# Kernel tuning notes

Measured on AMD Instinct MI355X. Metric: run time of the kernel, lower is better.

## Reference

```python
import jax, jax.numpy as jnp
import numpy as np

N_HEADS = 16
ROPE_THETA = 10000.0


def _rotate_half(x):
    d = x.shape[-1] // 2
    return jnp.concatenate([-x[..., d:], x[..., :d]], axis=-1)


def setup_inputs() -> dict:
    key = jax.random.key(0)
    k1, k2, k3, k4 = jax.random.split(key, 4)
    B, S, D = 2, 2048, 2048
    std = 0.02
    return {
        "x": jax.random.normal(k1, (B, S, D), dtype=jnp.float32),
        "wq": std * jax.random.normal(k2, (D, D), dtype=jnp.float32),
        "wkv": std * jax.random.normal(k3, (D, 2 * D), dtype=jnp.float32),
        "wo": std * jax.random.normal(k4, (D, D), dtype=jnp.float32),
    }


def reference(x, wq, wkv, wo):
    # prefill case: kv_cache=None, past_length=0
    B, S, D = x.shape
    H = N_HEADS
    dh = D // H

    Q = x @ wq.T                                   # [B,S,D]
    K, V = jnp.split(x @ wkv, 2, axis=-1)          # [B,S,D] each

    q = Q.reshape(B, S, H, dh).transpose(0, 2, 1, 3)  # [B,H,S,dh]
    k = K.reshape(B, S, H, dh).transpose(0, 2, 1, 3)
    v = V.reshape(B, S, H, dh).transpose(0, 2, 1, 3)

    # RoPE tables (cos/sin of outer(pos, inv_freq), duplicated across halves)
    inv_freq = 1.0 / (ROPE_THETA ** (jnp.arange(0, dh, 2, dtype=jnp.float32) / dh))
    emb = jnp.arange(S, dtype=jnp.float32)[:, None] * inv_freq[None, :]  # [S, dh/2]
    cos = jnp.tile(jnp.cos(emb), (1, 2))[None, None]  # [1,1,S,dh]
    sin = jnp.tile(jnp.sin(emb), (1, 2))[None, None]

    q = q * cos + _rotate_half(q) * sin
    k = k * cos + _rotate_half(k) * sin

    scale = 1.0 / jnp.sqrt(jnp.asarray(dh, dtype=x.dtype))
    scores = jnp.einsum('bhqd,bhkd->bhqk', q, k) * scale  # [B,H,S,S]
    causal = jnp.tril(jnp.ones((S, S), dtype=bool))
    scores = jnp.where(causal[None, None], scores, -jnp.inf)
    attn = jax.nn.softmax(scores, axis=-1)

    out = jnp.einsum('bhqk,bhkd->bhqd', attn, v)          # [B,H,S,dh]
    out = out.transpose(0, 2, 1, 3).reshape(B, S, D)
    return out @ wo.T
```

## Files before the change

kernel.cpp:

```cpp
#include <hip/hip_runtime.h>
#include <stdint.h>

typedef unsigned short u16;
typedef __attribute__((ext_vector_type(8))) short short8;
typedef __attribute__((ext_vector_type(4))) float floatx4;

#define MFMA16(a, b, c) __builtin_amdgcn_mfma_f32_16x16x32_bf16(a, b, c, 0, 0, 0)

static __device__ __forceinline__ void gl_lds16(const void* g, void* l) {
  __builtin_amdgcn_global_load_lds(
      (const __attribute__((address_space(1))) uint32_t*)g,
      (__attribute__((address_space(3))) uint32_t*)l, 16, 0, 0);
}

static __device__ __forceinline__ float b2f(u16 u) {
  union { float f; unsigned u; } v;
  v.u = ((unsigned)u) << 16;
  return v.f;
}
static __device__ __forceinline__ u16 f2b(float f) {
  union { float f; unsigned u; } v;
  v.f = f;
  unsigned r = v.u + 0x7fffu + ((v.u >> 16) & 1u);
  return (u16)(r >> 16);
}

template <int CTRL>
static __device__ __forceinline__ float dppf(float x) {
  return __builtin_bit_cast(
      float, __builtin_amdgcn_update_dpp(0, __builtin_bit_cast(int, x), CTRL,
                                         0xF, 0xF, true));
}
static __device__ __forceinline__ float sum16(float x) {
  x += dppf<0x128>(x);
  x += dppf<0x124>(x);
  x += dppf<0x122>(x);
  x += dppf<0x121>(x);
  return x;
}
static __device__ __forceinline__ float max16(float x) {
  x = fmaxf(x, dppf<0x128>(x));
  x = fmaxf(x, dppf<0x124>(x));
  x = fmaxf(x, dppf<0x122>(x));
  x = fmaxf(x, dppf<0x121>(x));
  return x;
}

__global__ __launch_bounds__(256) void detect_f32(const u16* __restrict__ x,
                                                  int* __restrict__ flag) {
  __shared__ int cnt[256];
  int c = 0;
  for (int i = threadIdx.x; i < 65536; i += 256) {
    int e = (x[i] >> 7) & 0xFF;
    if (e >= 140) ++c;
  }
  cnt[threadIdx.x] = c;
  __syncthreads();
  for (int s = 128; s > 0; s >>= 1) {
    if (threadIdx.x < (unsigned)s) cnt[threadIdx.x] += cnt[threadIdx.x + s];
    __syncthreads();
  }
  if (threadIdx.x == 0) *flag = (cnt[0] > 1000) ? 1 : 0;
}

__global__ __launch_bounds__(256) void convert_in8(const void* __restrict__ src,
                                                   u16* __restrict__ dst, int n8,
                                                   const int* __restrict__ flag) {
  int i = blockIdx.x * 256 + threadIdx.x;
  if (i >= n8) return;
  short8 r;
  if (*flag) {
    const float4* s = (const float4*)src;
    float4 a = s[2 * i], b = s[2 * i + 1];
    r[0] = (short)f2b(a.x); r[1] = (short)f2b(a.y);
    r[2] = (short)f2b(a.z); r[3] = (short)f2b(a.w);
    r[4] = (short)f2b(b.x); r[5] = (short)f2b(b.y);
    r[6] = (short)f2b(b.z); r[7] = (short)f2b(b.w);
  } else {
    r = ((const short8*)src)[i];
  }
  ((short8*)dst)[i] = r;
}

__global__ __launch_bounds__(256) void transpose_conv(const void* __restrict__ in,
                                                      u16* __restrict__ out,
                                                      int R, int Ccols,
                                                      const int* __restrict__ flag) {
  __shared__ u16 tile[32][33];
  int f = *flag;
  int c0 = blockIdx.x * 32, r0 = blockIdx.y * 32;
  int lx = threadIdx.x & 31, ly = threadIdx.x >> 5;
#pragma unroll
  for (int i = 0; i < 32; i += 8) {
    size_t idx = (size_t)(r0 + ly + i) * Ccols + c0 + lx;
    tile[ly + i][lx] = f ? f2b(((const float*)in)[idx]) : ((const u16*)in)[idx];
  }
  __syncthreads();
#pragma unroll
  for (int i = 0; i < 32; i += 8)
    out[(size_t)(c0 + ly + i) * R + r0 + lx] = tile[lx][ly + i];
}

__global__ __launch_bounds__(256) void transpose_v(const u16* __restrict__ KV,
                                                   u16* __restrict__ Vt) {
  __shared__ u16 tile[32][33];
  int b = blockIdx.z;
  int d0 = blockIdx.x * 32, s0 = blockIdx.y * 32;
  int lx = threadIdx.x & 31, ly = threadIdx.x >> 5;
  const u16* src = KV + ((size_t)(b * 2048 + s0)) * 4096 + 2048 + d0;
#pragma unroll
  for (int i = 0; i < 32; i += 8)
    tile[ly + i][lx] = src[(size_t)(ly + i) * 4096 + lx];
  __syncthreads();
  u16* dst = Vt + ((size_t)(b * 2048 + d0)) * 2048 + s0;
#pragma unroll
  for (int i = 0; i < 32; i += 8)
    dst[(size_t)(ly + i) * 2048 + lx] = tile[lx][ly + i];
}

__global__ __launch_bounds__(256) void gemm_nt(const u16* __restrict__ A,
                                               const u16* __restrict__ Bm,
                                               void* __restrict__ Cv,
                                               int M, int N, int K,
                                               const int* __restrict__ flag,
                                               int flag_mode) {
  __shared__ u16 Ash[128 * 64];
  __shared__ u16 Bsh[128 * 64];
  int tid = threadIdx.x, w = tid >> 6, lane = tid & 63;
  int quad = lane >> 4, l15 = lane & 15;
  int m0 = blockIdx.y * 128, n0 = blockIdx.x * 128;
  int wm = (w & 1) * 64, wn = (w >> 1) * 64;
  int f32out = flag_mode ? *flag : 0;

  floatx4 acc[4][4];
#pragma unroll
  for (int i = 0; i < 4; ++i)
#pragma unroll
    for (int j = 0; j < 4; ++j) acc[i][j] = floatx4{0.f, 0.f, 0.f, 0.f};

  int srow = lane >> 3;
  int gch = (lane & 7) ^ srow;
  const u16* Ag = A + (size_t)(m0 + w * 32 + srow) * K + gch * 8;
  const u16* Bg = Bm + (size_t)(n0 + w * 32 + srow) * K + gch * 8;

  for (int k0 = 0; k0 < K; k0 += 64) {
    __syncthreads();
#pragma unroll
    for (int t = 0; t < 4; ++t) {
      gl_lds16(Ag + (size_t)t * 8 * K + k0, (void*)(Ash + (w * 32 + t * 8) * 64));
      gl_lds16(Bg + (size_t)t * 8 * K + k0, (void*)(Bsh + (w * 32 + t * 8) * 64));
    }
    __syncthreads();
#pragma unroll
    for (int kk = 0; kk < 2; ++kk) {
      int c = kk * 4 + quad;
      short8 af[4], bf[4];
#pragma unroll
      for (int i = 0; i < 4; ++i) {
        int m = wm + 16 * i + l15;
        af[i] = *(const short8*)(Ash + m * 64 + ((c ^ (m & 7)) << 3));
        int n = wn + 16 * i + l15;
        bf[i] = *(const short8*)(Bsh + n * 64 + ((c ^ (n & 7)) << 3));
      }
#pragma unroll
      for (int i = 0; i < 4; ++i)
#pragma unroll
        for (int j = 0; j < 4; ++j) acc[i][j] = MFMA16(af[i], bf[j], acc[i][j]);
    }
  }

#pragma unroll
  for (int i = 0; i < 4; ++i)
#pragma unroll
    for (int r = 0; r < 4; ++r) {
      int row = m0 + wm + 16 * i + quad * 4 + r;
      if (f32out) {
        float* cp = (float*)Cv + (size_t)row * N + n0 + wn + l15;
#pragma unroll
        for (int j = 0; j < 4; ++j) cp[16 * j] = acc[i][j][r];
      } else {
        u16* cp = (u16*)Cv + (size_t)row * N + n0 + wn + l15;
#pragma unroll
        for (int j = 0; j < 4; ++j) cp[16 * j] = f2b(acc[i][j][r]);
      }
    }
}

__global__ __launch_bounds__(512, 2) void gemm8(const u16* __restrict__ A,
                                                const u16* __restrict__ Bm,
                                                void* __restrict__ Cv,
                                                int M, int N, int K,
                                                const int* __restrict__ flag,
                                                int flag_mode) {
  __shared__ u16 Ash[2 * 256 * 64];
  __shared__ u16 Bsh[2 * 256 * 64];
  int tid = threadIdx.x, w = tid >> 6, lane = tid & 63;
  int quad = lane >> 4, l15 = lane & 15;
  int wr = w >> 2, wc = w & 3;
  int wm = wr * 128, wn = wc * 64;
  int m0 = blockIdx.y * 256, n0 = blockIdx.x * 256;
  int f32out = flag_mode ? *flag : 0;
  const int NT = K >> 6;

  int srow8 = lane >> 3;
  int gch = (lane & 7) ^ srow8;
  const u16* Ag = A + (size_t)(m0 + w * 8 + srow8) * K + gch * 8;
  const u16* Bg = Bm + (size_t)(n0 + w * 8 + srow8) * K + gch * 8;
  int ldsrow = w * 8;

  floatx4 acc[8][4];
#pragma unroll
  for (int i = 0; i < 8; ++i)
#pragma unroll
    for (int j = 0; j < 4; ++j) acc[i][j] = floatx4{0.f, 0.f, 0.f, 0.f};

  int ch0 = ((quad ^ (l15 & 7)) << 3);
  int ch1 = (((4 + quad) ^ (l15 & 7)) << 3);

  auto stage = [&](int qi) {
    int tau = qi >> 2;
    int tc = tau < NT ? tau : NT - 1;
    int hh = qi & 3;
    int half = (hh & 1) * 128;
    int sbuf = (tau & 1) * (256 * 64);
    size_t kof = (size_t)tc * 64;
    if (hh < 2) {
      gl_lds16(Bg + (size_t)half * K + kof,
               (void*)(Bsh + sbuf + (half + ldsrow) * 64));
      gl_lds16(Bg + (size_t)(half + 64) * K + kof,
               (void*)(Bsh + sbuf + (half + 64 + ldsrow) * 64));
    } else {
      gl_lds16(Ag + (size_t)half * K + kof,
               (void*)(Ash + sbuf + (half + ldsrow) * 64));
      gl_lds16(Ag + (size_t)(half + 64) * K + kof,
               (void*)(Ash + sbuf + (half + 64 + ldsrow) * 64));
    }
  };

  stage(0); stage(1); stage(2); stage(3);
  __asm__ volatile("s_waitcnt vmcnt(4)" ::: "memory");
  stage(4); stage(5); stage(6);
  __asm__ volatile("s_waitcnt vmcnt(6)" ::: "memory");
  __builtin_amdgcn_s_barrier();

  for (int t = 0; t < NT; ++t) {
    u16* As = Ash + (t & 1) * (256 * 64);
    u16* Bs = Bsh + (t & 1) * (256 * 64);
    if (t) {
      __asm__ volatile("s_waitcnt vmcnt(6)" ::: "memory");
      __builtin_amdgcn_s_barrier();
    }
    int qb = 7 + 4 * t;
    short8 bf[8], af0[8], af1[8];

#pragma unroll
    for (int j = 0; j < 4; ++j) {
      int n = wn + 16 * j + l15;
      bf[2 * j] = *(const short8*)(Bs + n * 64 + ch0);
    }
#pragma unroll
    for (int i = 0; i < 4; ++i) {
      int m = wm + 16 * i + l15;
      af0[2 * i] = *(const short8*)(As + m * 64 + ch0);
    }
    stage(qb);
    __builtin_amdgcn_s_barrier();
    __asm__ volatile("s_waitcnt lgkmcnt(0)" ::: "memory");
    __builtin_amdgcn_sched_barrier(0);
    __builtin_amdgcn_s_setprio(1);
#pragma unroll
    for (int i = 0; i < 4; ++i)
#pragma unroll
      for (int j = 0; j < 4; ++j)
        acc[i][j] = MFMA16(af0[2 * i], bf[2 * j], acc[i][j]);
    __builtin_amdgcn_s_setprio(0);
    __builtin_amdgcn_s_barrier();

#pragma unroll
    for (int j = 0; j < 4; ++j) {
      int n = wn + 16 * j + l15;
      bf[2 * j + 1] = *(const short8*)(Bs + n * 64 + ch1);
    }
#pragma unroll
    for (int i = 0; i < 4; ++i) {
      int m = wm + 16 * i + l15;
      af0[2 * i + 1] = *(const short8*)(As + m * 64 + ch1);
    }
    stage(qb + 1);
    __builtin_amdgcn_s_barrier();
    __asm__ volatile("s_waitcnt lgkmcnt(0)" ::: "memory");
    __builtin_amdgcn_sched_barrier(0);
    __builtin_amdgcn_s_setprio(1);
#pragma unroll
    for (int i = 0; i < 4; ++i)
#pragma unroll
      for (int j = 0; j < 4; ++j)
        acc[i][j] = MFMA16(af0[2 * i + 1], bf[2 * j + 1], acc[i][j]);
    __builtin_amdgcn_s_setprio(0);
    __builtin_amdgcn_s_barrier();

#pragma unroll
    for (int i = 0; i < 4; ++i) {
      int m = wm + 64 + 16 * i + l15;
      af1[2 * i] = *(const short8*)(As + m * 64 + ch0);
    }
    stage(qb + 2);
    __builtin_amdgcn_s_barrier();
    __asm__ volatile("s_waitcnt lgkmcnt(0)" ::: "memory");
    __builtin_amdgcn_sched_barrier(0);
    __builtin_amdgcn_s_setprio(1);
#pragma unroll
    for (int i = 0; i < 4; ++i)
#pragma unroll
      for (int j = 0; j < 4; ++j)
        acc[4 + i][j] = MFMA16(af1[2 * i], bf[2 * j], acc[4 + i][j]);
    __builtin_amdgcn_s_setprio(0);
    __builtin_amdgcn_s_barrier();

#pragma unroll
    for (int i = 0; i < 4; ++i) {
      int m = wm + 64 + 16 * i + l15;
      af1[2 * i + 1] = *(const short8*)(As + m * 64 + ch1);
    }
    stage(qb + 3);
    __builtin_amdgcn_s_barrier();
    __asm__ volatile("s_waitcnt lgkmcnt(0)" ::: "memory");
    __builtin_amdgcn_sched_barrier(0);
    __builtin_amdgcn_s_setprio(1);
#pragma unroll
    for (int i = 0; i < 4; ++i)
#pragma unroll
      for (int j = 0; j < 4; ++j)
        acc[4 + i][j] = MFMA16(af1[2 * i + 1], bf[2 * j + 1], acc[4 + i][j]);
    __builtin_amdgcn_s_setprio(0);
    __builtin_amdgcn_s_barrier();
  }

#pragma unroll
  for (int i = 0; i < 8; ++i)
#pragma unroll
    for (int r = 0; r < 4; ++r) {
      int row = m0 + wm + 16 * i + quad * 4 + r;
      if (f32out) {
        float* cp = (float*)Cv + (size_t)row * N + n0 + wn + l15;
#pragma unroll
        for (int j = 0; j < 4; ++j) cp[16 * j] = acc[i][j][r];
      } else {
        u16* cp = (u16*)Cv + (size_t)row * N + n0 + wn + l15;
#pragma unroll
        for (int j = 0; j < 4; ++j) cp[16 * j] = f2b(acc[i][j][r]);
      }
    }
}

__global__ __launch_bounds__(256) void rope_kernel(u16* __restrict__ Q,
                                                   u16* __restrict__ KV) {
  const float scale = 0.08838834764831845f;
  int idx = blockIdx.x * 256 + threadIdx.x;
  int tok = idx >> 10;
  int rem = idx & 1023;
  int h = rem >> 6, i = rem & 63;
  int pos = tok & 2047;
  float f = __powf(10000.0f, -(float)(2 * i) * (1.0f / 128.0f));
  float ang = (float)pos * f;
  float s, c;
  sincosf(ang, &s, &c);

  size_t qb = (size_t)tok * 2048 + h * 128 + i;
  float q1 = b2f(Q[qb]), q2 = b2f(Q[qb + 64]);
  Q[qb] = f2b((q1 * c - q2 * s) * scale);
  Q[qb + 64] = f2b((q2 * c + q1 * s) * scale);

  size_t kb = (size_t)tok * 4096 + h * 128 + i;
  float k1 = b2f(KV[kb]), k2 = b2f(KV[kb + 64]);
  KV[kb] = f2b(k1 * c - k2 * s);
  KV[kb + 64] = f2b(k2 * c + k1 * s);
}

__global__ __launch_bounds__(512, 1) void flash_attn(const u16* __restrict__ Q,
                                                     const u16* __restrict__ KV,
                                                     const u16* __restrict__ Vt,
                                                     u16* __restrict__ O) {
  const int S = 2048, D = 2048, KVld = 4096;
  int bh = blockIdx.x;
  int pair = blockIdx.y;
  int b = bh >> 4, h = bh & 15;
  int tid = threadIdx.x, w = tid >> 6, lane = tid & 63;
  int quad = lane >> 4, l15 = lane & 15;

  const u16* Qb = Q + (size_t)(b * S) * D + h * 128;
  const u16* Kb = KV + (size_t)(b * S) * KVld + h * 128;
  const u16* Vtb = Vt + ((size_t)(b * 2048 + h * 128)) * S;

  __shared__ u16 Ksh[2][64 * 128];
  __shared__ u16 Vsh[2][128 * 64];
  __shared__ u16 Psh[8][16 * 64];

  auto stage_kv = [&](int kt, int buf) {
    int kb = kt * 64;
#pragma unroll
    for (int tt = 0; tt < 2; ++tt) {
      int r0 = w * 8 + tt * 4;
      int row = r0 + quad;
      int g = (l15 & 8) | ((l15 & 7) ^ (row & 7));
      gl_lds16(Kb + (size_t)(kb + row) * KVld + g * 8,
               (void*)(Ksh[buf] + r0 * 128));
    }
#pragma unroll
    for (int tt = 0; tt < 2; ++tt) {
      int d0 = w * 16 + tt * 8;
      int d = d0 + (lane >> 3);
      int g = (lane & 7) ^ (d & 7);
      gl_lds16(Vtb + (size_t)d * S + kb + g * 8, (void*)(Vsh[buf] + d0 * 64));
    }
  };

  for (int pi = 0; pi < 2; ++pi) {
    int qt = pi ? (15 - pair) : pair;
    int q0 = qt * 128;
    int qw = q0 + w * 16;

    short8 qf[4];
    {
      const u16* qp = Qb + (size_t)(qw + l15) * D + quad * 8;
#pragma unroll
      for (int kk = 0; kk < 4; ++kk) qf[kk] = *(const short8*)(qp + kk * 32);
    }

    floatx4 o[8];
#pragma unroll
    for (int t = 0; t < 8; ++t) o[t] = floatx4{0.f, 0.f, 0.f, 0.f};
    float mrow[4], lrow[4];
#pragma unroll
    for (int r = 0; r < 4; ++r) { mrow[r] = -1e30f; lrow[r] = 0.f; }

    int nk = 2 * qt + 2;
    stage_kv(0, 0);
    __syncthreads();

    for (int kt = 0; kt < nk; ++kt) {
      int kb = kt * 64;
      int cur = kt & 1;
      if (kt + 1 < nk) stage_kv(kt + 1, cur ^ 1);

      if (kb <= qw + 15) {
        const u16* Kc = Ksh[cur];
        const u16* Vc = Vsh[cur];
        floatx4 sc[4];
#pragma unroll
        for (int nf = 0; nf < 4; ++nf) sc[nf] = floatx4{0.f, 0.f, 0.f, 0.f};
#pragma unroll
        for (int kk = 0; kk < 4; ++kk) {
          int c = kk * 4 + quad;
          short8 kf[4];
#pragma unroll
          for (int nf = 0; nf < 4; ++nf) {
            int n = nf * 16 + l15;
            int pc = (c & 8) | ((c & 7) ^ (n & 7));
            kf[nf] = *(const short8*)(Kc + n * 128 + pc * 8);
          }
#pragma unroll
          for (int nf = 0; nf < 4; ++nf) sc[nf] = MFMA16(qf[kk], kf[nf], sc[nf]);
        }

        bool masked = (kb + 63 > qw);
        floatx4 alv;
#pragma unroll
        for (int r = 0; r < 4; ++r) {
          int qg = qw + quad * 4 + r;
          float v0 = sc[0][r], v1 = sc[1][r];
          float v2 = sc[2][r], v3 = sc[3][r];
          if (masked) {
            v0 = (kb + l15 <= qg) ? v0 : -1e30f;
            v1 = (kb + 16 + l15 <= qg) ? v1 : -1e30f;
            v2 = (kb + 32 + l15 <= qg) ? v2 : -1e30f;
            v3 = (kb + 48 + l15 <= qg) ? v3 : -1e30f;
          }
          float mx = max16(fmaxf(fmaxf(v0, v1), fmaxf(v2, v3)));
          float mn = fmaxf(mrow[r], mx);
          float al = __expf(mrow[r] - mn);
          mrow[r] = mn;
          float p0 = __expf(v0 - mn), p1 = __expf(v1 - mn);
          float p2 = __expf(v2 - mn), p3 = __expf(v3 - mn);
          float rs = sum16((p0 + p1) + (p2 + p3));
          lrow[r] = lrow[r] * al + rs;
          alv[r] = al;
          int m_ = quad * 4 + r;
          int sw = (m_ & 3) ^ ((m_ >> 2) << 1);
          int cb = l15 >> 3, e = l15 & 7;
          u16* pr = Psh[w] + m_ * 64;
          pr[(((0 + cb) ^ sw) << 3) + e] = f2b(p0);
          pr[(((2 + cb) ^ sw) << 3) + e] = f2b(p1);
          pr[(((4 + cb) ^ sw) << 3) + e] = f2b(p2);
          pr[(((6 + cb) ^ sw) << 3) + e] = f2b(p3);
        }
#pragma unroll
        for (int t = 0; t < 8; ++t) o[t] *= alv;
        __asm__ volatile("s_waitcnt lgkmcnt(0)" ::: "memory");

#pragma unroll
        for (int ks = 0; ks < 2; ++ks) {
          int c = ks * 4 + quad;
          int psw = (l15 & 3) ^ ((l15 >> 2) << 1);
          short8 pf = *(const short8*)(Psh[w] + l15 * 64 + ((c ^ psw) << 3));
#pragma unroll
          for (int t = 0; t < 8; ++t) {
            int d = t * 16 + l15;
            short8 vf = *(const short8*)(Vc + d * 64 + ((c ^ (d & 7)) << 3));
            o[t] = MFMA16(pf, vf, o[t]);
          }
        }
      }
      __syncthreads();
    }

#pragma unroll
    for (int r = 0; r < 4; ++r) {
      float inv = 1.0f / lrow[r];
      int qg = qw + quad * 4 + r;
      u16* op = O + (size_t)(b * S + qg) * D + h * 128;
#pragma unroll
      for (int t = 0; t < 8; ++t) op[t * 16 + l15] = f2b(o[t][r] * inv);
    }
  }
}

extern "C" void kernel_launch(void* const* d_in, const int* in_sizes, int n_in,
                              void* d_out, int out_size, void* d_ws, size_t ws_size,
                              hipStream_t stream) {
  const void* x = d_in[0];
  const void* wq = d_in[1];
  const void* wkv = d_in[2];
  const void* wo = d_in[3];

  int* flag = (int*)d_ws;
  u16* xb = (u16*)d_ws + 64;
  u16* Wbuf = xb + (size_t)8388608;
  u16* Qb = Wbuf + (size_t)8388608;
  u16* KVb = Qb + (size_t)8388608;
  u16* AO = xb;

  detect_f32<<<1, 256, 0, stream>>>((const u16*)x, flag);
  convert_in8<<<4096, 256, 0, stream>>>(x, xb, 1048576, flag);
  convert_in8<<<2048, 256, 0, stream>>>(wq, Wbuf, 524288, flag);
  gemm_nt<<<dim3(16, 32), 256, 0, stream>>>(xb, Wbuf, Qb, 4096, 2048, 2048, flag, 0);
  transpose_conv<<<dim3(128, 64), 256, 0, stream>>>(wkv, Wbuf, 2048, 4096, flag);
  gemm8<<<dim3(16, 16), 512, 0, stream>>>(xb, Wbuf, KVb, 4096, 4096, 2048, flag, 0);
  transpose_v<<<dim3(64, 64, 2), 256, 0, stream>>>(KVb, Wbuf);
  rope_kernel<<<16384, 256, 0, stream>>>(Qb, KVb);
  flash_attn<<<dim3(32, 8), 512, 0, stream>>>(Qb, KVb, Wbuf, AO);
  convert_in8<<<2048, 256, 0, stream>>>(wo, Wbuf, 524288, flag);
  gemm_nt<<<dim3(16, 32), 256, 0, stream>>>(AO, Wbuf, d_out, 4096, 2048, 2048, flag, 1);
}
```

Before: 476.9 us.

## Replace simple NT GEMM with pipelined 256x128 tile GEMM; skip unneeded rescale in attention

```diff
diff --git a/kernel.cpp b/kernel.cpp
--- a/kernel.cpp
+++ b/kernel.cpp
@@ -23,6 +23,11 @@
   v.f = f;
   unsigned r = v.u + 0x7fffu + ((v.u >> 16) & 1u);
   return (u16)(r >> 16);
+}
+static __device__ __forceinline__ u16 f2b_rn(float f) {
+  union { float f; unsigned u; } v;
+  v.f = f;
+  return (u16)((v.u + 0x8000u) >> 16);
 }
 
 template <int CTRL>
@@ -118,74 +123,6 @@
     dst[(size_t)(ly + i) * 2048 + lx] = tile[lx][ly + i];
 }
 
-__global__ __launch_bounds__(256) void gemm_nt(const u16* __restrict__ A,
-                                               const u16* __restrict__ Bm,
-                                               void* __restrict__ Cv,
-                                               int M, int N, int K,
-                                               const int* __restrict__ flag,
-                                               int flag_mode) {
-  __shared__ u16 Ash[128 * 64];
-  __shared__ u16 Bsh[128 * 64];
-  int tid = threadIdx.x, w = tid >> 6, lane = tid & 63;
-  int quad = lane >> 4, l15 = lane & 15;
-  int m0 = blockIdx.y * 128, n0 = blockIdx.x * 128;
-  int wm = (w & 1) * 64, wn = (w >> 1) * 64;
-  int f32out = flag_mode ? *flag : 0;
-
-  floatx4 acc[4][4];
-#pragma unroll
-  for (int i = 0; i < 4; ++i)
-#pragma unroll
-    for (int j = 0; j < 4; ++j) acc[i][j] = floatx4{0.f, 0.f, 0.f, 0.f};
-
-  int srow = lane >> 3;
-  int gch = (lane & 7) ^ srow;
-  const u16* Ag = A + (size_t)(m0 + w * 32 + srow) * K + gch * 8;
-  const u16* Bg = Bm + (size_t)(n0 + w * 32 + srow) * K + gch * 8;
-
-  for (int k0 = 0; k0 < K; k0 += 64) {
-    __syncthreads();
-#pragma unroll
-    for (int t = 0; t < 4; ++t) {
-      gl_lds16(Ag + (size_t)t * 8 * K + k0, (void*)(Ash + (w * 32 + t * 8) * 64));
-      gl_lds16(Bg + (size_t)t * 8 * K + k0, (void*)(Bsh + (w * 32 + t * 8) * 64));
-    }
-    __syncthreads();
-#pragma unroll
-    for (int kk = 0; kk < 2; ++kk) {
-      int c = kk * 4 + quad;
-      short8 af[4], bf[4];
-#pragma unroll
-      for (int i = 0; i < 4; ++i) {
-        int m = wm + 16 * i + l15;
-        af[i] = *(const short8*)(Ash + m * 64 + ((c ^ (m & 7)) << 3));
-        int n = wn + 16 * i + l15;
-        bf[i] = *(const short8*)(Bsh + n * 64 + ((c ^ (n & 7)) << 3));
-      }
-#pragma unroll
-      for (int i = 0; i < 4; ++i)
-#pragma unroll
-        for (int j = 0; j < 4; ++j) acc[i][j] = MFMA16(af[i], bf[j], acc[i][j]);
-    }
-  }
-
-#pragma unroll
-  for (int i = 0; i < 4; ++i)
-#pragma unroll
-    for (int r = 0; r < 4; ++r) {
-      int row = m0 + wm + 16 * i + quad * 4 + r;
-      if (f32out) {
-        float* cp = (float*)Cv + (size_t)row * N + n0 + wn + l15;
-#pragma unroll
-        for (int j = 0; j < 4; ++j) cp[16 * j] = acc[i][j][r];
-      } else {
-        u16* cp = (u16*)Cv + (size_t)row * N + n0 + wn + l15;
-#pragma unroll
-        for (int j = 0; j < 4; ++j) cp[16 * j] = f2b(acc[i][j][r]);
-      }
-    }
-}
-
 __global__ __launch_bounds__(512, 2) void gemm8(const u16* __restrict__ A,
                                                 const u16* __restrict__ Bm,
                                                 void* __restrict__ Cv,
@@ -353,6 +290,171 @@
     }
 }
 
+__global__ __launch_bounds__(512, 2) void gemm8n(const u16* __restrict__ A,
+                                                 const u16* __restrict__ Bm,
+                                                 void* __restrict__ Cv,
+                                                 int M, int N, int K,
+                                                 const int* __restrict__ flag,
+                                                 int flag_mode) {
+  __shared__ u16 Ash[2 * 256 * 64];
+  __shared__ u16 Bsh[2 * 128 * 64];
+  int tid = threadIdx.x, w = tid >> 6, lane = tid & 63;
+  int quad = lane >> 4, l15 = lane & 15;
+  int wr = w >> 2, wc = w & 3;
+  int wm = wr * 128, wn = wc * 32;
+  int m0 = blockIdx.y * 256, n0 = blockIdx.x * 128;
+  int f32out = flag_mode ? *flag : 0;
+  const int NT = K >> 6;
+
+  int srow8 = lane >> 3;
+  int gch = (lane & 7) ^ srow8;
+  const u16* Ag = A + (size_t)(m0 + w * 8 + srow8) * K + gch * 8;
+  const u16* Bg = Bm + (size_t)(n0 + w * 8 + srow8) * K + gch * 8;
+  int ldsrow = w * 8;
+
+  floatx4 acc[8][2];
+#pragma unroll
+  for (int i = 0; i < 8; ++i)
+#pragma unroll
+    for (int j = 0; j < 2; ++j) acc[i][j] = floatx4{0.f, 0.f, 0.f, 0.f};
+
+  int ch0 = ((quad ^ (l15 & 7)) << 3);
+  int ch1 = (((4 + quad) ^ (l15 & 7)) << 3);
+
+  auto stage = [&](int qi) {
+    int tau = qi / 3;
+    int tc = tau < NT ? tau : NT - 1;
+    int ss = qi - 3 * tau;
+    size_t kof = (size_t)tc * 64;
+    if (ss == 0) {
+      int sB = (tau & 1) * (128 * 64);
+      gl_lds16(Bg + kof, (void*)(Bsh + sB + ldsrow * 64));
+      gl_lds16(Bg + (size_t)64 * K + kof,
+               (void*)(Bsh + sB + (64 + ldsrow) * 64));
+    } else {
+      int sA = (tau & 1) * (256 * 64);
+      int half = (ss - 1) * 128;
+      gl_lds16(Ag + (size_t)half * K + kof,
+               (void*)(Ash + sA + (half + ldsrow) * 64));
+      gl_lds16(Ag + (size_t)(half + 64) * K + kof,
+               (void*)(Ash + sA + (half + 64 + ldsrow) * 64));
+    }
+  };
+
+  stage(0); stage(1); stage(2);
+  stage(3); stage(4);
+  __asm__ volatile("s_waitcnt vmcnt(4)" ::: "memory");
+  __builtin_amdgcn_s_barrier();
+
+  for (int t = 0; t < NT; ++t) {
+    u16* As = Ash + (t & 1) * (256 * 64);
+    u16* Bs = Bsh + (t & 1) * (128 * 64);
+    if (t) {
+      __asm__ volatile("s_waitcnt vmcnt(4)" ::: "memory");
+      __builtin_amdgcn_s_barrier();
+    }
+    int qb = 5 + 3 * t;
+    short8 bf[4], af0[8], af1[8];
+
+#pragma unroll
+    for (int j = 0; j < 2; ++j) {
+      int n = wn + 16 * j + l15;
+      bf[2 * j] = *(const short8*)(Bs + n * 64 + ch0);
+    }
+#pragma unroll
+    for (int i = 0; i < 4; ++i) {
+      int m = wm + 16 * i + l15;
+      af0[2 * i] = *(const short8*)(As + m * 64 + ch0);
+    }
+    stage(qb);
+    __builtin_amdgcn_s_barrier();
+    __asm__ volatile("s_waitcnt lgkmcnt(0)" ::: "memory");
+    __builtin_amdgcn_sched_barrier(0);
+    __builtin_amdgcn_s_setprio(1);
+#pragma unroll
+    for (int i = 0; i < 4; ++i)
+#pragma unroll
+      for (int j = 0; j < 2; ++j)
+        acc[i][j] = MFMA16(af0[2 * i], bf[2 * j], acc[i][j]);
+    __builtin_amdgcn_s_setprio(0);
+    __builtin_amdgcn_s_barrier();
+
+#pragma unroll
+    for (int j = 0; j < 2; ++j) {
+      int n = wn + 16 * j + l15;
+      bf[2 * j + 1] = *(const short8*)(Bs + n * 64 + ch1);
+    }
+#pragma unroll
+    for (int i = 0; i < 4; ++i) {
+      int m = wm + 16 * i + l15;
+      af0[2 * i + 1] = *(const short8*)(As + m * 64 + ch1);
+    }
+    stage(qb + 1);
+    __builtin_amdgcn_s_barrier();
+    __asm__ volatile("s_waitcnt lgkmcnt(0)" ::: "memory");
+    __builtin_amdgcn_sched_barrier(0);
+    __builtin_amdgcn_s_setprio(1);
+#pragma unroll
+    for (int i = 0; i < 4; ++i)
+#pragma unroll
+      for (int j = 0; j < 2; ++j)
+        acc[i][j] = MFMA16(af0[2 * i + 1], bf[2 * j + 1], acc[i][j]);
+    __builtin_amdgcn_s_setprio(0);
+    __builtin_amdgcn_s_barrier();
+
+#pragma unroll
+    for (int i = 0; i < 4; ++i) {
+      int m = wm + 64 + 16 * i + l15;
+      af1[2 * i] = *(const short8*)(As + m * 64 + ch0);
+    }
+    __builtin_amdgcn_s_barrier();
+    __asm__ volatile("s_waitcnt lgkmcnt(0)" ::: "memory");
+    __builtin_amdgcn_sched_barrier(0);
+    __builtin_amdgcn_s_setprio(1);
+#pragma unroll
+    for (int i = 0; i < 4; ++i)
+#pragma unroll
+      for (int j = 0; j < 2; ++j)
+        acc[4 + i][j] = MFMA16(af1[2 * i], bf[2 * j], acc[4 + i][j]);
+    __builtin_amdgcn_s_setprio(0);
+    __builtin_amdgcn_s_barrier();
+
+#pragma unroll
+    for (int i = 0; i < 4; ++i) {
+      int m = wm + 64 + 16 * i + l15;
+      af1[2 * i + 1] = *(const short8*)(As + m * 64 + ch1);
+    }
+    stage(qb + 2);
+    __builtin_amdgcn_s_barrier();
+    __asm__ volatile("s_waitcnt lgkmcnt(0)" ::: "memory");
+    __builtin_amdgcn_sched_barrier(0);
+    __builtin_amdgcn_s_setprio(1);
+#pragma unroll
+    for (int i = 0; i < 4; ++i)
+#pragma unroll
+      for (int j = 0; j < 2; ++j)
+        acc[4 + i][j] = MFMA16(af1[2 * i + 1], bf[2 * j + 1], acc[4 + i][j]);
+    __builtin_amdgcn_s_setprio(0);
+    __builtin_amdgcn_s_barrier();
+  }
+
+#pragma unroll
+  for (int i = 0; i < 8; ++i)
+#pragma unroll
+    for (int r = 0; r < 4; ++r) {
+      int row = m0 + wm + 16 * i + quad * 4 + r;
+      if (f32out) {
+        float* cp = (float*)Cv + (size_t)row * N + n0 + wn + l15;
+#pragma unroll
+        for (int j = 0; j < 2; ++j) cp[16 * j] = acc[i][j][r];
+      } else {
+        u16* cp = (u16*)Cv + (size_t)row * N + n0 + wn + l15;
+#pragma unroll
+        for (int j = 0; j < 2; ++j) cp[16 * j] = f2b(acc[i][j][r]);
+      }
+    }
+}
+
 __global__ __launch_bounds__(256) void rope_kernel(u16* __restrict__ Q,
                                                    u16* __restrict__ KV) {
   const float scale = 0.08838834764831845f;
@@ -417,8 +519,7 @@
 
   for (int pi = 0; pi < 2; ++pi) {
     int qt = pi ? (15 - pair) : pair;
-    int q0 = qt * 128;
-    int qw = q0 + w * 16;
+    int qw = qt * 128 + w * 16;
 
     short8 qf[4];
     {
@@ -489,13 +590,16 @@
           int sw = (m_ & 3) ^ ((m_ >> 2) << 1);
           int cb = l15 >> 3, e = l15 & 7;
           u16* pr = Psh[w] + m_ * 64;
-          pr[(((0 + cb) ^ sw) << 3) + e] = f2b(p0);
-          pr[(((2 + cb) ^ sw) << 3) + e] = f2b(p1);
-          pr[(((4 + cb) ^ sw) << 3) + e] = f2b(p2);
-          pr[(((6 + cb) ^ sw) << 3) + e] = f2b(p3);
+          pr[(((0 + cb) ^ sw) << 3) + e] = f2b_rn(p0);
+          pr[(((2 + cb) ^ sw) << 3) + e] = f2b_rn(p1);
+          pr[(((4 + cb) ^ sw) << 3) + e] = f2b_rn(p2);
+          pr[(((6 + cb) ^ sw) << 3) + e] = f2b_rn(p3);
         }
-#pragma unroll
-        for (int t = 0; t < 8; ++t) o[t] *= alv;
+        if (__any((alv[0] != 1.f) || (alv[1] != 1.f) ||
+                  (alv[2] != 1.f) || (alv[3] != 1.f))) {
+#pragma unroll
+          for (int t = 0; t < 8; ++t) o[t] *= alv;
+        }
         __asm__ volatile("s_waitcnt lgkmcnt(0)" ::: "memory");
 
 #pragma unroll
@@ -543,12 +647,12 @@
   detect_f32<<<1, 256, 0, stream>>>((const u16*)x, flag);
   convert_in8<<<4096, 256, 0, stream>>>(x, xb, 1048576, flag);
   convert_in8<<<2048, 256, 0, stream>>>(wq, Wbuf, 524288, flag);
-  gemm_nt<<<dim3(16, 32), 256, 0, stream>>>(xb, Wbuf, Qb, 4096, 2048, 2048, flag, 0);
+  gemm8n<<<dim3(16, 16), 512, 0, stream>>>(xb, Wbuf, Qb, 4096, 2048, 2048, flag, 0);
   transpose_conv<<<dim3(128, 64), 256, 0, stream>>>(wkv, Wbuf, 2048, 4096, flag);
   gemm8<<<dim3(16, 16), 512, 0, stream>>>(xb, Wbuf, KVb, 4096, 4096, 2048, flag, 0);
   transpose_v<<<dim3(64, 64, 2), 256, 0, stream>>>(KVb, Wbuf);
   rope_kernel<<<16384, 256, 0, stream>>>(Qb, KVb);
   flash_attn<<<dim3(32, 8), 512, 0, stream>>>(Qb, KVb, Wbuf, AO);
   convert_in8<<<2048, 256, 0, stream>>>(wo, Wbuf, 524288, flag);
-  gemm_nt<<<dim3(16, 32), 256, 0, stream>>>(AO, Wbuf, d_out, 4096, 2048, 2048, flag, 1);
-}
+  gemm8n<<<dim3(16, 16), 512, 0, stream>>>(AO, Wbuf, d_out, 4096, 2048, 2048, flag, 1);
+}
```

New measurement: 494.0 us. +3.6%, slower.
